# Performance work log

Hardware: AMD Instinct MI355X
Metric: run time of the kernel (lower is better)

Reference implementation:

```python
import jax, jax.numpy as jnp
import numpy as np

NG, NL, NCAM, NP, ED = 8, 4, 6, 7, 256  # groups, levels, cams, key points, embed dims
GD = ED // NG
FIX_SCALE = jnp.array([[0.0, 0.0, 0.0], [0.45, 0.0, 0.0], [-0.45, 0.0, 0.0],
                       [0.0, 0.45, 0.0], [0.0, -0.45, 0.0], [0.0, 0.0, 0.45],
                       [0.0, 0.0, -0.45]], dtype=jnp.float32)


def grid_sample_bilinear(feat, grid):
    """feat [N,C,H,W], grid [N,A,P,2] in [-1,1]; bilinear, zeros padding, align_corners=False."""
    N, C, H, W = feat.shape
    A, P = grid.shape[1], grid.shape[2]
    gx = (grid[..., 0] + 1.0) * (W * 0.5) - 0.5
    gy = (grid[..., 1] + 1.0) * (H * 0.5) - 0.5
    x0 = jnp.floor(gx)
    y0 = jnp.floor(gy)
    wx1 = gx - x0
    wy1 = gy - y0
    feat_flat = feat.reshape(N, C, H * W)

    def gather(xi, yi, w):
        valid = (xi >= 0) & (xi <= W - 1) & (yi >= 0) & (yi <= H - 1)
        xc = jnp.clip(xi, 0, W - 1).astype(jnp.int32)
        yc = jnp.clip(yi, 0, H - 1).astype(jnp.int32)
        idx = (yc * W + xc).reshape(N, 1, A * P)
        vals = jnp.take_along_axis(feat_flat, idx, axis=2)  # [N,C,A*P]
        return vals * (w * valid).reshape(N, 1, A * P)

    out = (gather(x0, y0, (1.0 - wx1) * (1.0 - wy1))
           + gather(x0 + 1.0, y0, wx1 * (1.0 - wy1))
           + gather(x0, y0 + 1.0, (1.0 - wx1) * wy1)
           + gather(x0 + 1.0, y0 + 1.0, wx1 * wy1))
    return out.reshape(N, C, A, P)


def _forward(instance_feature, anchor, anchor_embed, feat0, feat1, feat2, feat3,
             projection_mat, image_wh, w_fc, b_fc, w_out, b_out):
    B, A = anchor.shape[:2]
    # --- key point generation (box_code_size=8: size + yaw rotation + translation) ---
    size = jnp.exp(anchor[..., 3:6])[:, :, None, :]           # [B,A,1,3]
    kp = FIX_SCALE * size                                      # [B,A,7,3]
    sin, cos = anchor[..., 6], anchor[..., 7]
    z = jnp.zeros_like(cos)
    o = jnp.ones_like(cos)
    rot = jnp.stack([jnp.stack([cos, -sin, z], -1),
                     jnp.stack([sin, cos, z], -1),
                     jnp.stack([z, z, o], -1)], -2)            # [B,A,3,3]
    kp = jnp.einsum('baij,bapj->bapi', rot, kp) + anchor[..., None, 0:3]

    # --- attention weights: softmax over cams*levels*pts per group ---
    feature = instance_feature + anchor_embed
    w = feature @ w_fc.T + b_fc                                # [B,A,NG*NCAM*NL*NP]
    w = jax.nn.softmax(w.reshape(B, A, NCAM * NL * NP, NG), axis=2)
    w = w.reshape(B, A, NCAM, NL, NP, NG)

    # --- project key points to normalized image coords ---
    pts = jnp.concatenate([kp, jnp.ones_like(kp[..., :1])], -1)  # [B,A,7,4]
    p2d = jnp.einsum('bcij,bapj->bcapi', projection_mat, pts)[..., :3]
    xy = p2d[..., :2] / jnp.maximum(p2d[..., 2:3], 1e-5)
    xy = xy / jnp.maximum(image_wh[:, :, None, None], 1e-5)
    grid = (xy * 2.0 - 1.0).reshape(B * NCAM, A, NP, 2)

    # --- multilevel bilinear sampling ---
    levels = [feat0, feat1, feat2, feat3]
    sampled = jnp.stack([grid_sample_bilinear(f.reshape((B * NCAM,) + f.shape[2:]), grid)
                         for f in levels], axis=1)             # [B*Ncam,NL,C,A,P]
    feats = sampled.reshape(B, NCAM, NL, ED, A, NP).transpose(0, 4, 1, 2, 5, 3)  # [B,A,Ncam,NL,P,C]
    feats = feats.reshape(B, A, NCAM, NL, NP, NG, GD)

    # --- weighted fusion over cams, levels, then sum over key points ---
    fused = jnp.einsum('bacnpgd,bacnpg->bagd', feats, w).reshape(B, A, ED)
    return fused @ w_out.T + b_out


def setup_inputs() -> dict:
    ks = jax.random.split(jax.random.key(0), 13)
    B, A = 2, 900
    return {
        'instance_feature': jax.random.normal(ks[0], (B, A, ED), jnp.float32),
        'anchor': jax.random.normal(ks[1], (B, A, 8), jnp.float32),
        'anchor_embed': jax.random.normal(ks[2], (B, A, ED), jnp.float32),
        'feat0': jax.random.normal(ks[3], (B, NCAM, ED, 64, 176), jnp.float32),
        'feat1': jax.random.normal(ks[4], (B, NCAM, ED, 32, 88), jnp.float32),
        'feat2': jax.random.normal(ks[5], (B, NCAM, ED, 16, 44), jnp.float32),
        'feat3': jax.random.normal(ks[6], (B, NCAM, ED, 8, 22), jnp.float32),
        'projection_mat': jax.random.normal(ks[7], (B, NCAM, 4, 4), jnp.float32),
        'image_wh': jnp.ones((B, NCAM, 2), jnp.float32),
        'w_fc': jax.random.normal(ks[8], (NG * NCAM * NL * NP, ED), jnp.float32) * 0.02,
        'b_fc': jax.random.normal(ks[9], (NG * NCAM * NL * NP,), jnp.float32) * 0.02,
        'w_out': jax.random.normal(ks[10], (ED, ED), jnp.float32) * 0.02,
        'b_out': jax.random.normal(ks[11], (ED,), jnp.float32) * 0.02,
    }


def reference(instance_feature, anchor, anchor_embed, feat0, feat1, feat2, feat3,
              projection_mat, image_wh, w_fc, b_fc, w_out, b_out):
    return _forward(instance_feature, anchor, anchor_embed, feat0, feat1, feat2, feat3,
                    projection_mat, image_wh, w_fc, b_fc, w_out, b_out)
```

## Files before the change

### kernel.cpp

```cpp
#include <hip/hip_runtime.h>
#include <math.h>

constexpr int B = 2, A = 900, ED = 256, NG = 8, NCAM = 6, NL = 4, NP = 7;
constexpr int NJ = NG * NCAM * NL * NP;
constexpr int NBA = B * A;
constexpr int NE = NCAM * NL * NP;
constexpr int LDST = 260;
constexpr int SPLIT = 2;
constexpr int EHALF = NE / SPLIT;

__constant__ float FIXS[NP][3] = {
  {0.f,0.f,0.f},{0.45f,0.f,0.f},{-0.45f,0.f,0.f},
  {0.f,0.45f,0.f},{0.f,-0.45f,0.f},{0.f,0.f,0.45f},{0.f,0.f,-0.45f}};

__constant__ int cH[NL]  = {64,32,16,8};
__constant__ int cW[NL]  = {176,88,44,22};
__constant__ int cHW[NL] = {11264,2816,704,176};
__constant__ long long cLOFF[NL] = {0LL, 0LL, 8650752LL, 10813440LL};

__global__ __launch_bounds__(256) void k_tr_cl(
    const float* __restrict__ f1, const float* __restrict__ f2,
    const float* __restrict__ f3, float* __restrict__ tfeat)
{
  __shared__ float tile[32 * LDST];
  const int bc = blockIdx.y;
  const int bx = blockIdx.x;
  int lvl, t0;
  if      (bx < 88)  { lvl = 1; t0 = 0; }
  else if (bx < 110) { lvl = 2; t0 = 88; }
  else               { lvl = 3; t0 = 110; }
  const int HW  = cHW[lvl];
  const int px0 = (bx - t0) * 32;
  const float* in = ((lvl==1)?f1:(lvl==2)?f2:f3) + (size_t)bc * ED * HW + px0;
  float* outp = tfeat + cLOFF[lvl] + ((size_t)bc * HW + px0) * ED;
  const int t = threadIdx.x;
  const int npx = min(32, HW - px0);

#pragma unroll
  for (int j = 0; j < 8; ++j) {
    const int px = 4 * j;
    if (px < npx) {
      const float4 v = *(const float4*)(in + (size_t)t * HW + px);
      tile[(px+0)*LDST + t] = v.x;
      tile[(px+1)*LDST + t] = v.y;
      tile[(px+2)*LDST + t] = v.z;
      tile[(px+3)*LDST + t] = v.w;
    }
  }
  __syncthreads();
  const int wv = t >> 6, l = t & 63;
  for (int px = wv; px < npx; px += 4) {
    const float4 v = *(const float4*)&tile[px*LDST + 4*l];
    *(float4*)(outp + (size_t)px * ED + 4*l) = v;
  }
}

__global__ __launch_bounds__(256) void k_tr(const float* __restrict__ in,
                                            float* __restrict__ out, int R, int C)
{
  __shared__ float tile[32][33];
  const int r0 = blockIdx.y * 32, c0 = blockIdx.x * 32;
  const int tx = threadIdx.x, ty = threadIdx.y;
#pragma unroll
  for (int kk = 0; kk < 4; ++kk) {
    const int r = r0 + ty + kk*8, c = c0 + tx;
    if (r < R && c < C) tile[ty + kk*8][tx] = in[(size_t)r*C + c];
  }
  __syncthreads();
#pragma unroll
  for (int kk = 0; kk < 4; ++kk) {
    const int c = c0 + ty + kk*8, r = r0 + tx;
    if (r < R && c < C) out[(size_t)c*R + r] = tile[tx][ty + kk*8];
  }
}

__global__ __launch_bounds__(192) void k_fc(const float* __restrict__ inst,
    const float* __restrict__ emb, const float* __restrict__ wt,
    const float* __restrict__ b_fc, float* __restrict__ wraw)
{
  __shared__ float fsh[8][ED];
  const int a0 = blockIdx.x * 8;
  const int j  = blockIdx.y * 192 + threadIdx.x;
  const int t  = threadIdx.x;

  for (int i = t; i < 8 * ED; i += 192) {
    const int a = i >> 8, k = i & 255;
    const size_t idx = (size_t)(a0 + a) * ED + k;
    fsh[a][k] = inst[idx] + emb[idx];
  }
  __syncthreads();

  float acc[8] = {0.f,0.f,0.f,0.f,0.f,0.f,0.f,0.f};
  for (int k = 0; k < ED; k += 4) {
    float w0 = wt[(size_t)(k+0)*NJ + j];
    float w1 = wt[(size_t)(k+1)*NJ + j];
    float w2 = wt[(size_t)(k+2)*NJ + j];
    float w3 = wt[(size_t)(k+3)*NJ + j];
#pragma unroll
    for (int a = 0; a < 8; ++a)
      acc[a] += w0*fsh[a][k] + w1*fsh[a][k+1] + w2*fsh[a][k+2] + w3*fsh[a][k+3];
  }
  const float bj = b_fc[j];
#pragma unroll
  for (int a = 0; a < 8; ++a)
    wraw[(size_t)(a0+a)*NJ + j] = acc[a] + bj;
}

template<bool CL>
__global__ __launch_bounds__(256) void k_sample_h(
    const float* __restrict__ anchor, const float* __restrict__ proj,
    const float* __restrict__ wh, const float* __restrict__ wraw,
    const float* __restrict__ tfeat,
    const float* __restrict__ f0, const float* __restrict__ f1,
    const float* __restrict__ f2, const float* __restrict__ f3,
    float* __restrict__ fused)
{
  __shared__ float wsh[NJ];
  __shared__ float gridsh[NCAM][NP][2];
  __shared__ const float* cptr[EHALF][4];
  __shared__ float4 cwt[EHALF];
  __shared__ int2   cmeta[EHALF];
  __shared__ int wcnt[4];

  const int ba   = blockIdx.x;
  const int half = blockIdx.y;
  const int b    = ba / A;
  const int t    = threadIdx.x;

  for (int j = t; j < NJ; j += 256)
    wsh[(j & 7) * NE + (j >> 3)] = wraw[(size_t)ba*NJ + j];

  if (t < NCAM*NP) {
    const int c = t / NP, p = t % NP;
    const float* an = anchor + (size_t)ba * 8;
    const float sx = expf(an[3]), sy = expf(an[4]), sz = expf(an[5]);
    const float sn = an[6], cs = an[7];
    const float kx = FIXS[p][0]*sx, ky = FIXS[p][1]*sy, kz = FIXS[p][2]*sz;
    const float px = cs*kx - sn*ky + an[0];
    const float py = sn*kx + cs*ky + an[1];
    const float pz = kz + an[2];
    const float* P = proj + ((size_t)(b*NCAM + c))*16;
    const float X = P[0]*px + P[1]*py + P[2]*pz  + P[3];
    const float Y = P[4]*px + P[5]*py + P[6]*pz  + P[7];
    const float Z = P[8]*px + P[9]*py + P[10]*pz + P[11];
    const float zc  = fmaxf(Z, 1e-5f);
    const float whx = fmaxf(wh[(b*NCAM+c)*2+0], 1e-5f);
    const float why = fmaxf(wh[(b*NCAM+c)*2+1], 1e-5f);
    gridsh[c][p][0] = (X/zc/whx)*2.f - 1.f;
    gridsh[c][p][1] = (Y/zc/why)*2.f - 1.f;
  }
  __syncthreads();

  bool valid = false;
  int chstep = 0;
  float4 w4 = make_float4(0.f,0.f,0.f,0.f);
  const float *p00=nullptr, *p10=nullptr, *p01=nullptr, *p11=nullptr;
  const int e = half * EHALF + t;
  if (t < EHALF) {
    const int c = e / (NL*NP); const int r = e % (NL*NP);
    const int l = r / NP, p = r % NP;
    const int Wl = cW[l], Hl = cH[l], HWl = cHW[l];
    const float gx = (gridsh[c][p][0] + 1.f) * (Wl * 0.5f) - 0.5f;
    const float gy = (gridsh[c][p][1] + 1.f) * (Hl * 0.5f) - 0.5f;
    const float x0f = floorf(gx), y0f = floorf(gy);
    const bool vx0 = (x0f >=  0.f) & (x0f <= (float)(Wl-1));
    const bool vx1 = (x0f >= -1.f) & (x0f <= (float)(Wl-2));
    const bool vy0 = (y0f >=  0.f) & (y0f <= (float)(Hl-1));
    const bool vy1 = (y0f >= -1.f) & (y0f <= (float)(Hl-2));
    if (vx0|vx1|vy0|vy1) {
      const float wx1 = gx - x0f, wy1 = gy - y0f;
      const int x0 = (int)fmaxf(fminf(x0f,        (float)(Wl-1)), 0.f);
      const int x1 = (int)fmaxf(fminf(x0f + 1.f,  (float)(Wl-1)), 0.f);
      const int y0 = (int)fmaxf(fminf(y0f,        (float)(Hl-1)), 0.f);
      const int y1 = (int)fmaxf(fminf(y0f + 1.f,  (float)(Hl-1)), 0.f);
      w4 = make_float4((1.f-wx1)*(1.f-wy1)*(vx0&&vy0),
                       wx1*(1.f-wy1)*(vx1&&vy0),
                       (1.f-wx1)*wy1*(vx0&&vy1),
                       wx1*wy1*(vx1&&vy1));
      if (w4.x != 0.f || w4.y != 0.f || w4.z != 0.f || w4.w != 0.f) {
        const float* base;
        int estep;
        if (CL && l >= 1) {
          base = tfeat + cLOFF[l] + (size_t)(b*NCAM + c) * HWl * ED;
          estep = ED; chstep = 1;
        } else {
          const float* fp = (l==0)?f0:(l==1)?f1:(l==2)?f2:f3;
          base = fp + (size_t)(b*NCAM + c) * ED * HWl;
          estep = 1; chstep = HWl;
        }
        p00 = base + (size_t)(y0*Wl + x0) * estep;
        p10 = base + (size_t)(y0*Wl + x1) * estep;
        p01 = base + (size_t)(y1*Wl + x0) * estep;
        p11 = base + (size_t)(y1*Wl + x1) * estep;
        valid = true;
      }
    }
  }

  const unsigned long long mask = __ballot(valid);
  const int lane = t & 63, wv = t >> 6;
  if (lane == 0) wcnt[wv] = __popcll(mask);
  __syncthreads();
  int off = 0, nv = 0;
#pragma unroll
  for (int i = 0; i < 4; ++i) { if (i < wv) off += wcnt[i]; nv += wcnt[i]; }
  if (valid) {
    const int pos = off + __popcll(mask & ((1ull << lane) - 1ull));
    cptr[pos][0] = p00; cptr[pos][1] = p10; cptr[pos][2] = p01; cptr[pos][3] = p11;
    cwt[pos]   = w4;
    cmeta[pos] = make_int2(chstep, e);
  }

  {
    const int g = t >> 5, ln = t & 31;
    float* wg = wsh + g * NE;
    float m = -3.4e38f;
    for (int i = ln; i < NE; i += 32) m = fmaxf(m, wg[i]);
#pragma unroll
    for (int mk = 16; mk >= 1; mk >>= 1) m = fmaxf(m, __shfl_xor(m, mk));
    float s = 0.f;
    for (int i = ln; i < NE; i += 32) {
      const float ev = expf(wg[i] - m);
      wg[i] = ev;
      s += ev;
    }
#pragma unroll
    for (int mk = 16; mk >= 1; mk >>= 1) s += __shfl_xor(s, mk);
    const float inv = 1.f / s;
    for (int i = ln; i < NE; i += 32) wg[i] *= inv;
  }
  __syncthreads();

  float acc = 0.f;
  const int g = t >> 5;
#pragma unroll 4
  for (int i = 0; i < nv; ++i) {
    const int2 m = cmeta[i];
    const size_t toff = (size_t)t * m.x;
    const float4 w = cwt[i];
    const float aw = wsh[g*NE + m.y];
    const float v00 = cptr[i][0][toff];
    const float v10 = cptr[i][1][toff];
    const float v01 = cptr[i][2][toff];
    const float v11 = cptr[i][3][toff];
    acc += aw * (w.x*v00 + w.y*v10 + w.z*v01 + w.w*v11);
  }
  fused[((size_t)half * NBA + ba) * ED + t] = acc;
}

__global__ __launch_bounds__(256) void k_out(const float* __restrict__ fused,
    const float* __restrict__ w_out, const float* __restrict__ b_out,
    float* __restrict__ out)
{
  __shared__ float fsh[8][ED];
  const int a0 = blockIdx.x * 8;
  const int t = threadIdx.x;
#pragma unroll
  for (int k = 0; k < 8; ++k)
    fsh[k][t] = fused[(size_t)(a0+k)*ED + t]
              + fused[(size_t)NBA*ED + (size_t)(a0+k)*ED + t];
  __syncthreads();
  float acc[8] = {0.f,0.f,0.f,0.f,0.f,0.f,0.f,0.f};
  for (int i = 0; i < ED; i += 4) {
    const float4 w4 = *(const float4*)&w_out[(size_t)t*ED + i];
#pragma unroll
    for (int k = 0; k < 8; ++k) {
      const float4 fv = *(const float4*)&fsh[k][i];
      acc[k] += w4.x*fv.x + w4.y*fv.y + w4.z*fv.z + w4.w*fv.w;
    }
  }
  const float bo = b_out[t];
#pragma unroll
  for (int k = 0; k < 8; ++k) out[(size_t)(a0+k)*ED + t] = acc[k] + bo;
}

extern "C" void kernel_launch(void* const* d_in, const int* in_sizes, int n_in,
                              void* d_out, int out_size, void* d_ws, size_t ws_size,
                              hipStream_t stream) {
  const float* inst   = (const float*)d_in[0];
  const float* anchor = (const float*)d_in[1];
  const float* emb    = (const float*)d_in[2];
  const float* f0 = (const float*)d_in[3];
  const float* f1 = (const float*)d_in[4];
  const float* f2 = (const float*)d_in[5];
  const float* f3 = (const float*)d_in[6];
  const float* proj  = (const float*)d_in[7];
  const float* wh    = (const float*)d_in[8];
  const float* w_fc  = (const float*)d_in[9];
  const float* b_fc  = (const float*)d_in[10];
  const float* w_out = (const float*)d_in[11];
  const float* b_out = (const float*)d_in[12];
  float* out = (float*)d_out;
  float* ws  = (float*)d_ws;

  const size_t TFEAT = 11354112ULL;
  const size_t WRAW  = (size_t)NBA * NJ;
  const size_t FUSED = (size_t)SPLIT * NBA * ED;
  const size_t WT    = (size_t)ED * NJ;
  const bool tr = ws_size >= (TFEAT + WRAW + FUSED + WT) * sizeof(float);

  float* tfeat  = ws;
  float* wraw   = tr ? (ws + TFEAT) : ws;
  float* fusedp = wraw + WRAW;
  float* wt     = fusedp + FUSED;

  k_tr<<<dim3(ED/32, NJ/32, 1), dim3(32,8), 0, stream>>>(w_fc, wt, NJ, ED);

  if (tr)
    k_tr_cl<<<dim3(116, B*NCAM), 256, 0, stream>>>(f1, f2, f3, tfeat);

  k_fc<<<dim3(NBA / 8, 7), 192, 0, stream>>>(inst, emb, wt, b_fc, wraw);

  if (tr)
    k_sample_h<true><<<dim3(NBA, SPLIT), 256, 0, stream>>>(anchor, proj, wh,
        wraw, tfeat, f0, f1, f2, f3, fusedp);
  else
    k_sample_h<false><<<dim3(NBA, SPLIT), 256, 0, stream>>>(anchor, proj, wh,
        wraw, tfeat, f0, f1, f2, f3, fusedp);

  k_out<<<NBA / 8, 256, 0, stream>>>(fusedp, w_out, b_out, out);
}
```

Measured before the change: 365.4 us.

## Merge feature transpose and FC into one launch, drop weight transpose

Folds the channel-last feature transpose and the attention-weight FC into a single kernel whose blocks split by index between the two jobs. It also removes the separate w_fc transpose kernel: the FC now reads each weight row directly with float4 loads and uses 256-thread blocks (6 column blocks, the last partly idle). This saves two launches and lets the independent transpose and GEMM work overlap, but each thread now reads a strided row of w_fc instead of coalesced columns, which may hurt memory efficiency in the FC.

```diff
diff --git a/kernel.cpp b/kernel.cpp
--- a/kernel.cpp
+++ b/kernel.cpp
@@ -9,6 +9,10 @@
 constexpr int SPLIT = 2;
 constexpr int EHALF = NE / SPLIT;
 
+constexpr int NTRB = 116 * B * NCAM;
+constexpr int NFCJ = 6;
+constexpr int NFCB = (NBA / 8) * NFCJ;
+
 __constant__ float FIXS[NP][3] = {
   {0.f,0.f,0.f},{0.45f,0.f,0.f},{-0.45f,0.f,0.f},
   {0.f,0.45f,0.f},{0.f,-0.45f,0.f},{0.f,0.f,0.45f},{0.f,0.f,-0.45f}};
@@ -18,92 +22,76 @@
 __constant__ int cHW[NL] = {11264,2816,704,176};
 __constant__ long long cLOFF[NL] = {0LL, 0LL, 8650752LL, 10813440LL};
 
-__global__ __launch_bounds__(256) void k_tr_cl(
+__global__ __launch_bounds__(256) void k_prep(
     const float* __restrict__ f1, const float* __restrict__ f2,
-    const float* __restrict__ f3, float* __restrict__ tfeat)
+    const float* __restrict__ f3,
+    const float* __restrict__ inst, const float* __restrict__ emb,
+    const float* __restrict__ w_fc, const float* __restrict__ b_fc,
+    float* __restrict__ tfeat, float* __restrict__ wraw, int ntr)
 {
-  __shared__ float tile[32 * LDST];
-  const int bc = blockIdx.y;
-  const int bx = blockIdx.x;
-  int lvl, t0;
-  if      (bx < 88)  { lvl = 1; t0 = 0; }
-  else if (bx < 110) { lvl = 2; t0 = 88; }
-  else               { lvl = 3; t0 = 110; }
-  const int HW  = cHW[lvl];
-  const int px0 = (bx - t0) * 32;
-  const float* in = ((lvl==1)?f1:(lvl==2)?f2:f3) + (size_t)bc * ED * HW + px0;
-  float* outp = tfeat + cLOFF[lvl] + ((size_t)bc * HW + px0) * ED;
-  const int t = threadIdx.x;
-  const int npx = min(32, HW - px0);
-
-#pragma unroll
-  for (int j = 0; j < 8; ++j) {
-    const int px = 4 * j;
-    if (px < npx) {
-      const float4 v = *(const float4*)(in + (size_t)t * HW + px);
-      tile[(px+0)*LDST + t] = v.x;
-      tile[(px+1)*LDST + t] = v.y;
-      tile[(px+2)*LDST + t] = v.z;
-      tile[(px+3)*LDST + t] = v.w;
-    }
-  }
-  __syncthreads();
-  const int wv = t >> 6, l = t & 63;
-  for (int px = wv; px < npx; px += 4) {
-    const float4 v = *(const float4*)&tile[px*LDST + 4*l];
-    *(float4*)(outp + (size_t)px * ED + 4*l) = v;
-  }
-}
-
-__global__ __launch_bounds__(256) void k_tr(const float* __restrict__ in,
-                                            float* __restrict__ out, int R, int C)
-{
-  __shared__ float tile[32][33];
-  const int r0 = blockIdx.y * 32, c0 = blockIdx.x * 32;
-  const int tx = threadIdx.x, ty = threadIdx.y;
-#pragma unroll
-  for (int kk = 0; kk < 4; ++kk) {
-    const int r = r0 + ty + kk*8, c = c0 + tx;
-    if (r < R && c < C) tile[ty + kk*8][tx] = in[(size_t)r*C + c];
-  }
-  __syncthreads();
-#pragma unroll
-  for (int kk = 0; kk < 4; ++kk) {
-    const int c = c0 + ty + kk*8, r = r0 + tx;
-    if (r < R && c < C) out[(size_t)c*R + r] = tile[tx][ty + kk*8];
-  }
-}
-
-__global__ __launch_bounds__(192) void k_fc(const float* __restrict__ inst,
-    const float* __restrict__ emb, const float* __restrict__ wt,
-    const float* __restrict__ b_fc, float* __restrict__ wraw)
-{
-  __shared__ float fsh[8][ED];
-  const int a0 = blockIdx.x * 8;
-  const int j  = blockIdx.y * 192 + threadIdx.x;
-  const int t  = threadIdx.x;
-
-  for (int i = t; i < 8 * ED; i += 192) {
-    const int a = i >> 8, k = i & 255;
-    const size_t idx = (size_t)(a0 + a) * ED + k;
-    fsh[a][k] = inst[idx] + emb[idx];
-  }
-  __syncthreads();
-
-  float acc[8] = {0.f,0.f,0.f,0.f,0.f,0.f,0.f,0.f};
-  for (int k = 0; k < ED; k += 4) {
-    float w0 = wt[(size_t)(k+0)*NJ + j];
-    float w1 = wt[(size_t)(k+1)*NJ + j];
-    float w2 = wt[(size_t)(k+2)*NJ + j];
-    float w3 = wt[(size_t)(k+3)*NJ + j];
-#pragma unroll
-    for (int a = 0; a < 8; ++a)
-      acc[a] += w0*fsh[a][k] + w1*fsh[a][k+1] + w2*fsh[a][k+2] + w3*fsh[a][k+3];
-  }
-  const float bj = b_fc[j];
-#pragma unroll
-  for (int a = 0; a < 8; ++a)
-    wraw[(size_t)(a0+a)*NJ + j] = acc[a] + bj;
+  __shared__ float smem[32 * LDST];
+  const int bid = blockIdx.x;
+  const int t   = threadIdx.x;
+
+  if (bid < ntr) {
+    const int bc = bid / 116;
+    const int bx = bid % 116;
+    int lvl, t0;
+    if      (bx < 88)  { lvl = 1; t0 = 0; }
+    else if (bx < 110) { lvl = 2; t0 = 88; }
+    else               { lvl = 3; t0 = 110; }
+    const int HW  = cHW[lvl];
+    const int px0 = (bx - t0) * 32;
+    const float* in = ((lvl==1)?f1:(lvl==2)?f2:f3) + (size_t)bc * ED * HW + px0;
+    float* outp = tfeat + cLOFF[lvl] + ((size_t)bc * HW + px0) * ED;
+    const int npx = min(32, HW - px0);
+
+#pragma unroll
+    for (int j = 0; j < 8; ++j) {
+      const int px = 4 * j;
+      if (px < npx) {
+        const float4 v = *(const float4*)(in + (size_t)t * HW + px);
+        smem[(px+0)*LDST + t] = v.x;
+        smem[(px+1)*LDST + t] = v.y;
+        smem[(px+2)*LDST + t] = v.z;
+        smem[(px+3)*LDST + t] = v.w;
+      }
+    }
+    __syncthreads();
+    const int wv = t >> 6, l = t & 63;
+    for (int px = wv; px < npx; px += 4) {
+      const float4 v = *(const float4*)&smem[px*LDST + 4*l];
+      *(float4*)(outp + (size_t)px * ED + 4*l) = v;
+    }
+  } else {
+    const int fb = bid - ntr;
+    const int a0 = (fb / NFCJ) * 8;
+    const int j  = (fb % NFCJ) * 256 + t;
+    float* fsh = smem;
+
+    for (int i = t; i < 8 * ED; i += 256) {
+      const int a = i >> 8, k = i & 255;
+      const size_t idx = (size_t)(a0 + a) * ED + k;
+      fsh[a*ED + k] = inst[idx] + emb[idx];
+    }
+    __syncthreads();
+
+    if (j < NJ) {
+      float acc[8] = {0.f,0.f,0.f,0.f,0.f,0.f,0.f,0.f};
+      const float* wrow = w_fc + (size_t)j * ED;
+      for (int k = 0; k < ED; k += 4) {
+        const float4 w4 = *(const float4*)(wrow + k);
+#pragma unroll
+        for (int a = 0; a < 8; ++a)
+          acc[a] += w4.x*fsh[a*ED + k]   + w4.y*fsh[a*ED + k+1]
+                  + w4.z*fsh[a*ED + k+2] + w4.w*fsh[a*ED + k+3];
+      }
+      const float bj = b_fc[j];
+#pragma unroll
+      for (int a = 0; a < 8; ++a)
+        wraw[(size_t)(a0+a)*NJ + j] = acc[a] + bj;
+    }
+  }
 }
 
 template<bool CL>
@@ -296,20 +284,16 @@
   const size_t TFEAT = 11354112ULL;
   const size_t WRAW  = (size_t)NBA * NJ;
   const size_t FUSED = (size_t)SPLIT * NBA * ED;
-  const size_t WT    = (size_t)ED * NJ;
-  const bool tr = ws_size >= (TFEAT + WRAW + FUSED + WT) * sizeof(float);
+  const bool tr = ws_size >= (TFEAT + WRAW + FUSED) * sizeof(float);
 
   float* tfeat  = ws;
   float* wraw   = tr ? (ws + TFEAT) : ws;
   float* fusedp = wraw + WRAW;
-  float* wt     = fusedp + FUSED;
-
-  k_tr<<<dim3(ED/32, NJ/32, 1), dim3(32,8), 0, stream>>>(w_fc, wt, NJ, ED);
-
-  if (tr)
-    k_tr_cl<<<dim3(116, B*NCAM), 256, 0, stream>>>(f1, f2, f3, tfeat);
-
-  k_fc<<<dim3(NBA / 8, 7), 192, 0, stream>>>(inst, emb, wt, b_fc, wraw);
+
+  const int ntr = tr ? NTRB : 0;
+
+  k_prep<<<ntr + NFCB, 256, 0, stream>>>(f1, f2, f3, inst, emb, w_fc, b_fc,
+                                         tfeat, wraw, ntr);
 
   if (tr)
     k_sample_h<true><<<dim3(NBA, SPLIT), 256, 0, stream>>>(anchor, proj, wh,
```

Result: no change. 365.6 us (+0.0%).
